# Performance work log

Hardware: AMD Instinct MI355X
Metric: run time of the kernel (lower is better)

The kernel has to match this reference:

```python
import jax, jax.numpy as jnp
import numpy as np

N, D, H, R = 50000, 256, 4, 3
C = D // H        # head dim = 64
E = 400000        # edges per relation
NEG = 0.2         # LeakyReLU slope
LN_EPS = 1e-5


def _segment_softmax(att, seg, n):
    # att: [E, H], seg: [E] destination node ids -> softmax per (node, head)
    m = jax.ops.segment_max(att, seg, num_segments=n)
    m = jnp.where(jnp.isfinite(m), m, 0.0)        # nodes with no edges
    e = jnp.exp(att - m[seg])
    s = jax.ops.segment_sum(e, seg, num_segments=n)
    return e / (s[seg] + 1e-16)


def setup_inputs() -> dict:
    key = jax.random.key(0)
    ks = jax.random.split(key, 16)
    inp = {
        'feat': jax.random.normal(ks[0], (N, D), jnp.float32),
        'Wl': jax.random.normal(ks[1], (D, D), jnp.float32) / np.sqrt(D).astype(np.float32),
        'bl': jnp.zeros((D,), jnp.float32),
        'Wr': jax.random.normal(ks[2], (D, D), jnp.float32) / np.sqrt(D).astype(np.float32),
        'br': jnp.zeros((D,), jnp.float32),
        'attn_l': jax.random.normal(ks[3], (R, H, C), jnp.float32) / np.sqrt(C).astype(np.float32),
        'attn_r': jax.random.normal(ks[4], (R, H, C), jnp.float32) / np.sqrt(C).astype(np.float32),
        'rel_q': jax.random.normal(ks[5], (H, C), jnp.float32) / np.sqrt(C).astype(np.float32),
        'rel_k': jax.random.normal(ks[6], (H, C), jnp.float32) / np.sqrt(C).astype(np.float32),
        'ln_gamma': jnp.ones((D,), jnp.float32),
        'ln_beta': jnp.zeros((D,), jnp.float32),
    }
    for r in range(R):
        inp[f'edge_src_{r}'] = jax.random.randint(ks[7 + 2 * r], (E,), 0, N, jnp.int64 if jax.config.jax_enable_x64 else jnp.int32)
        inp[f'edge_dst_{r}'] = jax.random.randint(ks[8 + 2 * r], (E,), 0, N, jnp.int64 if jax.config.jax_enable_x64 else jnp.int32)
    return inp


def reference(feat, Wl, bl, Wr, br, attn_l, attn_r, rel_q, rel_k, ln_gamma, ln_beta,
              edge_src_0, edge_dst_0, edge_src_1, edge_dst_1, edge_src_2, edge_dst_2):
    # per-node-type linear projections -> multi-head [N, H, C]
    k = (feat @ Wl + bl).reshape(N, H, C)
    v = (feat @ Wr + br).reshape(N, H, C)
    srcs = [edge_src_0, edge_src_1, edge_src_2]
    dsts = [edge_dst_0, edge_dst_1, edge_dst_2]
    rel_outs = []
    for r in range(R):  # loop over fixed, structurally distinct relations
        s, d = srcs[r], dsts[r]
        # edge attention: (k_src . a_l) + (v_dst . a_r), LeakyReLU (attn_dropout inactive in eval)
        att = jnp.einsum('ehc,hc->eh', k[s], attn_l[r]) + jnp.einsum('ehc,hc->eh', v[d], attn_r[r])
        att = jax.nn.leaky_relu(att, NEG)
        a = _segment_softmax(att, d, N)                                   # [E, H]
        # message 'h' is edges.dst['v'] in the original code (faithful)
        h = jax.ops.segment_sum(a[:, :, None] * v[d], d, num_segments=N)  # [N, H, C]
        rel_outs.append(h)
    # stack relation embeddings + self 'v' (the +1 none-selection relation)
    x = jnp.stack(rel_outs + [v], axis=1)                                  # [N, T=R+1, H, C]
    # MetapathGATConv (1 layer) stand-in: self embedding queries all relations per head
    q = jnp.einsum('nhc,hc->nh', x[:, -1], rel_q)                          # [N, H]
    kk = jnp.einsum('nthc,hc->nth', x, rel_k)                              # [N, T, H]
    beta = jax.nn.softmax(jax.nn.leaky_relu(q[:, None, :] + kk, NEG), axis=1)  # [N, T, H]
    out = jnp.einsum('nth,nthc->nhc', beta, x).reshape(N, D)
    # activation -> (dropout inactive in eval) -> LayerNorm
    out = jax.nn.relu(out)
    mu = out.mean(-1, keepdims=True)
    var = out.var(-1, keepdims=True)
    out = (out - mu) * jax.lax.rsqrt(var + LN_EPS) * ln_gamma + ln_beta
    return out
```

## Files before the change

kernel.cpp:

```cpp
#include <hip/hip_runtime.h>

#define N_NODES 50000
#define DIM 256
#define NEG 0.2f
#define LN_EPS 1e-5f
#define SCAT_BLOCKS 2048

typedef __attribute__((ext_vector_type(8))) short short8;
typedef __attribute__((ext_vector_type(4))) float f32x4;

__device__ __forceinline__ unsigned short f2bf(float x) {
    unsigned int u = __builtin_bit_cast(unsigned int, x);
    u += 0x7fffu + ((u >> 16) & 1u);
    return (unsigned short)(u >> 16);
}

__device__ __forceinline__ void load_lds16(const void* g, void* l) {
    __builtin_amdgcn_global_load_lds((const unsigned int*)g, (unsigned int*)l, 16, 0, 0);
}

__global__ __launch_bounds__(256) void prep(
    const float* __restrict__ Wr, unsigned short* __restrict__ WrF,
    const int* __restrict__ d0, const int* __restrict__ d1, const int* __restrict__ d2,
    int E, unsigned char* __restrict__ mask)
{
    if (blockIdx.x < 32) {
        const int o    = blockIdx.x * 256 + threadIdx.x;
        const int lane = o & 63;
        const int frag = o >> 6;
        const int kk = frag & 7, mt = frag >> 3;
        const int ln = lane & 15, quad = lane >> 4;
        const float* src = Wr + (size_t)(kk * 32 + quad * 8) * DIM + mt * 16 + ln;
        short8 v;
        #pragma unroll
        for (int j = 0; j < 8; ++j) v[j] = (short)f2bf(src[(size_t)j * DIM]);
        *(short8*)(WrF + (size_t)o * 8) = v;
    } else {
        const int total = 3 * E;
        for (int i = (blockIdx.x - 32) * 256 + (int)threadIdx.x; i < total;
             i += SCAT_BLOCKS * 256) {
            const int* d; int base, e;
            if (i >= 2 * E)  { d = d2; e = i - 2 * E; base = 2 * N_NODES; }
            else if (i >= E) { d = d1; e = i - E;     base = N_NODES; }
            else             { d = d0; e = i;         base = 0; }
            mask[base + d[e]] = (unsigned char)1;
        }
    }
}

__global__ __launch_bounds__(256, 4) void fused_mfma(
    const float* __restrict__ feat, const unsigned short* __restrict__ WrF,
    const float* __restrict__ br, const float* __restrict__ rel_q,
    const float* __restrict__ rel_k, const float* __restrict__ gamma,
    const float* __restrict__ beta_p, const unsigned char* __restrict__ mask,
    float* __restrict__ out)
{
    __shared__ unsigned short lds[2][8192];
    const int lane = threadIdx.x & 63;
    const int wave = threadIdx.x >> 6;
    const int ln = lane & 15;
    const int quad = lane >> 4;
    int node = blockIdx.x * 64 + wave * 16 + ln;
    const bool valid = node < N_NODES;
    if (!valid) node = N_NODES - 1;

    {
        const char* g = (const char*)WrF;
        #pragma unroll
        for (int r = 0; r < 4; ++r) {
            const int off = wave * 4096 + r * 1024;
            load_lds16(g + off + lane * 16, (char*)lds[0] + off);
        }
    }

    const int m0 = (int)mask[node];
    const int m1 = (int)mask[N_NODES + node];
    const int m2 = (int)mask[2 * N_NODES + node];

    const float* fptr = feat + (size_t)node * DIM + quad * 8;
    float4 F0[8], F1[8];
    #pragma unroll
    for (int kk = 0; kk < 8; ++kk) {
        F0[kk] = *(const float4*)(fptr + kk * 32);
        F1[kk] = *(const float4*)(fptr + kk * 32 + 4);
    }
    short8 bfr[8];
    #pragma unroll
    for (int kk = 0; kk < 8; ++kk) {
        bfr[kk][0] = (short)f2bf(F0[kk].x); bfr[kk][1] = (short)f2bf(F0[kk].y);
        bfr[kk][2] = (short)f2bf(F0[kk].z); bfr[kk][3] = (short)f2bf(F0[kk].w);
        bfr[kk][4] = (short)f2bf(F1[kk].x); bfr[kk][5] = (short)f2bf(F1[kk].y);
        bfr[kk][6] = (short)f2bf(F1[kk].z); bfr[kk][7] = (short)f2bf(F1[kk].w);
    }

    f32x4 acc[16];
    #pragma unroll
    for (int mt = 0; mt < 16; ++mt) acc[mt] = (f32x4){0.f, 0.f, 0.f, 0.f};

    __syncthreads();

    #pragma unroll
    for (int p = 0; p < 8; ++p) {
        if (p < 7) {
            const char* g = (const char*)WrF + (p + 1) * 16384;
            char* l = (char*)lds[(p + 1) & 1];
            #pragma unroll
            for (int r = 0; r < 4; ++r) {
                const int off = wave * 4096 + r * 1024;
                load_lds16(g + off + lane * 16, l + off);
            }
        }
        const char* b = (const char*)lds[p & 1];
        #pragma unroll
        for (int kk = 0; kk < 8; ++kk) {
            #pragma unroll
            for (int mtl = 0; mtl < 2; ++mtl) {
                const short8 a = *(const short8*)(b + (mtl * 8 + kk) * 1024 + lane * 16);
                acc[p * 2 + mtl] =
                    __builtin_amdgcn_mfma_f32_16x16x32_bf16(a, bfr[kk], acc[p * 2 + mtl], 0, 0, 0);
            }
        }
        if (p < 7) __syncthreads();
    }

    float qp[4] = {0.f, 0.f, 0.f, 0.f}, kp[4] = {0.f, 0.f, 0.f, 0.f};
    #pragma unroll
    for (int mt = 0; mt < 16; ++mt) {
        const int cbase = mt * 16 + quad * 4;
        const float4 bb = *(const float4*)(br + cbase);
        acc[mt][0] += bb.x; acc[mt][1] += bb.y; acc[mt][2] += bb.z; acc[mt][3] += bb.w;
        const float4 rq = *(const float4*)(rel_q + cbase);
        const float4 rk = *(const float4*)(rel_k + cbase);
        const int h = mt >> 2;
        qp[h] += acc[mt][0] * rq.x + acc[mt][1] * rq.y + acc[mt][2] * rq.z + acc[mt][3] * rq.w;
        kp[h] += acc[mt][0] * rk.x + acc[mt][1] * rk.y + acc[mt][2] * rk.z + acc[mt][3] * rk.w;
    }
    #pragma unroll
    for (int h = 0; h < 4; ++h) {
        qp[h] += __shfl_xor(qp[h], 16); qp[h] += __shfl_xor(qp[h], 32);
        kp[h] += __shfl_xor(kp[h], 16); kp[h] += __shfl_xor(kp[h], 32);
    }

    const int cnt = m0 + m1 + m2;

    float wgt[4];
    #pragma unroll
    for (int h = 0; h < 4; ++h) {
        const float q = qp[h];
        const float qk = q + kp[h];
        const float a = q  > 0.f ? q  : NEG * q;
        const float b = qk > 0.f ? qk : NEG * qk;
        const float mx = fmaxf(a, b);
        const float eb = (float)(cnt + 1) * __expf(b - mx);
        const float ea = (float)(3 - cnt) * __expf(a - mx);
        wgt[h] = eb / (eb + ea);
    }

    float sum = 0.f, ssq = 0.f;
    #pragma unroll
    for (int mt = 0; mt < 16; ++mt) {
        const float w = wgt[mt >> 2];
        #pragma unroll
        for (int r = 0; r < 4; ++r) {
            float v = fmaxf(acc[mt][r] * w, 0.f);
            acc[mt][r] = v;
            sum += v; ssq += v * v;
        }
    }
    sum += __shfl_xor(sum, 16); sum += __shfl_xor(sum, 32);
    ssq += __shfl_xor(ssq, 16); ssq += __shfl_xor(ssq, 32);
    const float mu = sum * (1.f / 256.f);
    const float var = ssq * (1.f / 256.f) - mu * mu;
    const float rstd = rsqrtf(var + LN_EPS);

    if (valid) {
        float* optr = out + (size_t)node * DIM;
        #pragma unroll
        for (int mt = 0; mt < 16; ++mt) {
            const int cbase = mt * 16 + quad * 4;
            const float4 g = *(const float4*)(gamma + cbase);
            const float4 b = *(const float4*)(beta_p + cbase);
            float4 r;
            r.x = (acc[mt][0] - mu) * rstd * g.x + b.x;
            r.y = (acc[mt][1] - mu) * rstd * g.y + b.y;
            r.z = (acc[mt][2] - mu) * rstd * g.z + b.z;
            r.w = (acc[mt][3] - mu) * rstd * g.w + b.w;
            *(float4*)(optr + cbase) = r;
        }
    }
}

extern "C" void kernel_launch(void* const* d_in, const int* in_sizes, int n_in,
                              void* d_out, int out_size, void* d_ws, size_t ws_size,
                              hipStream_t stream) {
    const float* feat  = (const float*)d_in[0];
    const float* Wr    = (const float*)d_in[3];
    const float* br    = (const float*)d_in[4];
    const float* rel_q = (const float*)d_in[7];
    const float* rel_k = (const float*)d_in[8];
    const float* gamma = (const float*)d_in[9];
    const float* beta  = (const float*)d_in[10];
    const int* dst0 = (const int*)d_in[12];
    const int* dst1 = (const int*)d_in[14];
    const int* dst2 = (const int*)d_in[16];
    const int E = in_sizes[12];

    unsigned short* WrF = (unsigned short*)d_ws;
    unsigned char* mask = (unsigned char*)d_ws + DIM * DIM * 2;

    hipMemsetAsync(mask, 0, 150016, stream);
    prep<<<32 + SCAT_BLOCKS, 256, 0, stream>>>(Wr, WrF, dst0, dst1, dst2, E, mask);
    fused_mfma<<<(N_NODES + 63) / 64, 256, 0, stream>>>(
        feat, WrF, br, rel_q, rel_k, gamma, beta, mask, (float*)d_out);
}
```

Before: 182.8 us.

## Stream feature K-slices per stage and reorder weight fragments by K

The prepacked weight fragments are reordered so each pipeline stage holds one 32-wide K slice across all 16 output tiles, not all K for two output tiles. The feature row is then loaded and converted to bf16 one K slice at a time, double-buffered and prefetched two stages ahead, instead of loading the whole row up front. This is meant to cut register pressure from the 8 held B fragments and overlap feature loads with the MFMA work. The cost is a serial dependency of all 16 accumulators on each stage and tighter coupling between the packing layout and the loop order.

```diff
diff --git a/kernel.cpp b/kernel.cpp
--- a/kernel.cpp
+++ b/kernel.cpp
@@ -17,6 +17,15 @@
 
 __device__ __forceinline__ void load_lds16(const void* g, void* l) {
     __builtin_amdgcn_global_load_lds((const unsigned int*)g, (unsigned int*)l, 16, 0, 0);
+}
+
+__device__ __forceinline__ short8 cvt_bfrag(float4 a4, float4 b4) {
+    short8 r;
+    r[0] = (short)f2bf(a4.x); r[1] = (short)f2bf(a4.y);
+    r[2] = (short)f2bf(a4.z); r[3] = (short)f2bf(a4.w);
+    r[4] = (short)f2bf(b4.x); r[5] = (short)f2bf(b4.y);
+    r[6] = (short)f2bf(b4.z); r[7] = (short)f2bf(b4.w);
+    return r;
 }
 
 __global__ __launch_bounds__(256) void prep(
@@ -28,7 +37,7 @@
         const int o    = blockIdx.x * 256 + threadIdx.x;
         const int lane = o & 63;
         const int frag = o >> 6;
-        const int kk = frag & 7, mt = frag >> 3;
+        const int mt = frag & 15, kk = frag >> 4;
         const int ln = lane & 15, quad = lane >> 4;
         const float* src = Wr + (size_t)(kk * 32 + quad * 8) * DIM + mt * 16 + ln;
         short8 v;
@@ -64,6 +73,12 @@
     const bool valid = node < N_NODES;
     if (!valid) node = N_NODES - 1;
 
+    const float* fptr = feat + (size_t)node * DIM + quad * 8;
+
+    float4 FA[2], FB[2];
+    FA[0] = *(const float4*)(fptr);       FB[0] = *(const float4*)(fptr + 4);
+    FA[1] = *(const float4*)(fptr + 32);  FB[1] = *(const float4*)(fptr + 36);
+
     {
         const char* g = (const char*)WrF;
         #pragma unroll
@@ -77,25 +92,11 @@
     const int m1 = (int)mask[N_NODES + node];
     const int m2 = (int)mask[2 * N_NODES + node];
 
-    const float* fptr = feat + (size_t)node * DIM + quad * 8;
-    float4 F0[8], F1[8];
-    #pragma unroll
-    for (int kk = 0; kk < 8; ++kk) {
-        F0[kk] = *(const float4*)(fptr + kk * 32);
-        F1[kk] = *(const float4*)(fptr + kk * 32 + 4);
-    }
-    short8 bfr[8];
-    #pragma unroll
-    for (int kk = 0; kk < 8; ++kk) {
-        bfr[kk][0] = (short)f2bf(F0[kk].x); bfr[kk][1] = (short)f2bf(F0[kk].y);
-        bfr[kk][2] = (short)f2bf(F0[kk].z); bfr[kk][3] = (short)f2bf(F0[kk].w);
-        bfr[kk][4] = (short)f2bf(F1[kk].x); bfr[kk][5] = (short)f2bf(F1[kk].y);
-        bfr[kk][6] = (short)f2bf(F1[kk].z); bfr[kk][7] = (short)f2bf(F1[kk].w);
-    }
-
     f32x4 acc[16];
     #pragma unroll
     for (int mt = 0; mt < 16; ++mt) acc[mt] = (f32x4){0.f, 0.f, 0.f, 0.f};
+
+    short8 bcur = cvt_bfrag(FA[0], FB[0]);
 
     __syncthreads();
 
@@ -110,17 +111,20 @@
                 load_lds16(g + off + lane * 16, l + off);
             }
         }
+        if (p < 6) {
+            FA[p & 1] = *(const float4*)(fptr + (p + 2) * 32);
+            FB[p & 1] = *(const float4*)(fptr + (p + 2) * 32 + 4);
+        }
         const char* b = (const char*)lds[p & 1];
         #pragma unroll
-        for (int kk = 0; kk < 8; ++kk) {
-            #pragma unroll
-            for (int mtl = 0; mtl < 2; ++mtl) {
-                const short8 a = *(const short8*)(b + (mtl * 8 + kk) * 1024 + lane * 16);
-                acc[p * 2 + mtl] =
-                    __builtin_amdgcn_mfma_f32_16x16x32_bf16(a, bfr[kk], acc[p * 2 + mtl], 0, 0, 0);
-            }
-        }
-        if (p < 7) __syncthreads();
+        for (int mt = 0; mt < 16; ++mt) {
+            const short8 a = *(const short8*)(b + mt * 1024 + lane * 16);
+            acc[mt] = __builtin_amdgcn_mfma_f32_16x16x32_bf16(a, bcur, acc[mt], 0, 0, 0);
+        }
+        if (p < 7) {
+            bcur = cvt_bfrag(FA[(p + 1) & 1], FB[(p + 1) & 1]);
+            __syncthreads();
+        }
     }
 
     float qp[4] = {0.f, 0.f, 0.f, 0.f}, kp[4] = {0.f, 0.f, 0.f, 0.f};
```

Result: faster. 176.8 us (-3.3%).
